# Kernel tuning notes

Hardware: AMD Instinct MI355X
Metric: run time of the kernel (lower is better)

The kernel has to match this reference:

```python
import jax, jax.numpy as jnp
import numpy as np

LN_EPS = 1e-3  # keras LayerNormalization default epsilon


def setup_inputs() -> dict:
    key = jax.random.key(0)
    ks = jax.random.split(key, 6)
    B, S, D, H, K = 4, 4096, 1024, 16, 64
    scale = 1.0 / np.sqrt(D)
    return {
        "x": jax.random.normal(ks[0], (B, S, D), jnp.float32),
        "Wq": jax.random.normal(ks[1], (D, H, K), jnp.float32) * scale,
        "bq": jnp.zeros((H, K), jnp.float32),
        "Wk": jax.random.normal(ks[2], (D, H, K), jnp.float32) * scale,
        "bk": jnp.zeros((H, K), jnp.float32),
        "Wv": jax.random.normal(ks[3], (D, H, K), jnp.float32) * scale,
        "bv": jnp.zeros((H, K), jnp.float32),
        "Wo": jax.random.normal(ks[4], (H, K, D), jnp.float32) * scale,
        "bo": jnp.zeros((D,), jnp.float32),
        "gamma": jnp.ones((D,), jnp.float32),
        "beta": jnp.zeros((D,), jnp.float32),
        "num_window": 8,
    }


def reference(x, Wq, bq, Wk, bk, Wv, bv, Wo, bo, gamma, beta, num_window):
    B, S, D = x.shape
    H, K = Wq.shape[1], Wq.shape[2]
    Sw = S // num_window
    # Block-diagonal (windowed) attention: reshape seq into windows instead of a Python loop.
    xw = x.reshape(B, num_window, Sw, D)  # [B, W, Sw, D]
    q = jnp.einsum('bwsd,dhk->bwshk', xw, Wq) + bq
    k = jnp.einsum('bwsd,dhk->bwshk', xw, Wk) + bk
    v = jnp.einsum('bwsd,dhk->bwshk', xw, Wv) + bv
    scores = jnp.einsum('bwqhk,bwshk->bwhqs', q, k) / jnp.sqrt(jnp.asarray(K, x.dtype))
    attn = jax.nn.softmax(scores, axis=-1)  # [B, W, H, Sw, Sw]
    ctx = jnp.einsum('bwhqs,bwshk->bwqhk', attn, v)
    attn_out = (jnp.einsum('bwqhk,hkd->bwqd', ctx, Wo) + bo).reshape(B, S, D)
    # residual + layernorm (keras eps=1e-3)
    y = x + attn_out
    mu = jnp.mean(y, axis=-1, keepdims=True)
    var = jnp.mean(jnp.square(y - mu), axis=-1, keepdims=True)
    return (y - mu) * jax.lax.rsqrt(var + LN_EPS) * gamma + beta
```

## Files before the change

kernel.cpp:

```cpp
#include <hip/hip_runtime.h>

typedef __bf16 bf16_t;
typedef __bf16 bf16x4 __attribute__((ext_vector_type(4)));
typedef __bf16 bf16x8 __attribute__((ext_vector_type(8)));
typedef float f32x4 __attribute__((ext_vector_type(4)));
typedef float f32x16 __attribute__((ext_vector_type(16)));

#define MFMA16(a, b, c) __builtin_amdgcn_mfma_f32_16x16x32_bf16((a), (b), (c), 0, 0, 0)
#define MFMA32(a, b, c) __builtin_amdgcn_mfma_f32_32x32x16_bf16((a), (b), (c), 0, 0, 0)

__device__ __forceinline__ void gl_lds16(const bf16_t* g, bf16_t* l) {
  __builtin_amdgcn_global_load_lds(
      (const __attribute__((address_space(1))) void*)g,
      (__attribute__((address_space(3))) void*)l, 16, 0, 0);
}

__global__ __launch_bounds__(256) void cast_x_kernel(const float* __restrict__ x,
                                                     bf16_t* __restrict__ xb) {
  size_t i = (size_t)blockIdx.x * 256 + threadIdx.x;
  float4 v = ((const float4*)x)[i];
  bf16x4 o = {(bf16_t)v.x, (bf16_t)v.y, (bf16_t)v.z, (bf16_t)v.w};
  ((bf16x4*)xb)[i] = o;
}

__global__ __launch_bounds__(256) void transpose_w_kernel(
    const float* __restrict__ Wq, const float* __restrict__ Wk,
    const float* __restrict__ Wv, const float* __restrict__ Wo,
    bf16_t* __restrict__ Wt, bf16_t* __restrict__ WoT) {
  __shared__ bf16_t T[64 * 68];
  const int z = blockIdx.z;
  const float* src = (z == 0) ? Wq : (z == 1) ? Wk : (z == 2) ? Wv : Wo;
  bf16_t* dst = (z < 3) ? (Wt + (size_t)z * 1024 * 1024) : WoT;
  const int tr = blockIdx.y * 64;
  const int tc = blockIdx.x * 64;
  const int tid = threadIdx.x;
#pragma unroll
  for (int it = 0; it < 4; ++it) {
    int t = tid + it * 256;
    int row = t >> 4, c4 = t & 15;
    float4 v = *(const float4*)&src[(size_t)(tr + row) * 1024 + tc + c4 * 4];
    bf16x4 o = {(bf16_t)v.x, (bf16_t)v.y, (bf16_t)v.z, (bf16_t)v.w};
    *(bf16x4*)&T[row * 68 + c4 * 4] = o;
  }
  __syncthreads();
#pragma unroll
  for (int it = 0; it < 2; ++it) {
    int t = tid + it * 256;
    int n = t >> 3, d8 = t & 7;
    bf16x8 o;
#pragma unroll
    for (int j = 0; j < 8; ++j) o[j] = T[(d8 * 8 + j) * 68 + n];
    *(bf16x8*)&dst[(size_t)(tc + n) * 1024 + tr + d8 * 8] = o;
  }
}

__global__ __launch_bounds__(256) void gemm_qkv_kernel(
    const bf16_t* __restrict__ A, const bf16_t* __restrict__ Bt,
    const float* __restrict__ bq, const float* __restrict__ bk,
    const float* __restrict__ bv, bf16_t* __restrict__ C) {
  __shared__ bf16_t As[128 * 64];
  __shared__ bf16_t Bs[128 * 64];
  const int tid = threadIdx.x;
  const int bm = blockIdx.y, bn = blockIdx.x;
  const int lane = tid & 63;
  const int l31 = lane & 31, lh = lane >> 5;
  const int wv = tid >> 6;
  const int wm = (wv & 1) * 64, wn = (wv >> 1) * 64;

  f32x16 acc[2][2];
#pragma unroll
  for (int i = 0; i < 2; ++i)
#pragma unroll
    for (int j = 0; j < 2; ++j)
#pragma unroll
      for (int e = 0; e < 16; ++e) acc[i][j][e] = 0.f;

  const bf16_t* Abase = A + (size_t)(bm * 128) * 1024;
  const bf16_t* Bbase = Bt + (size_t)(bn * 128) * 1024;

  for (int kt = 0; kt < 16; ++kt) {
    const int k0 = kt * 64;
#pragma unroll
    for (int i = 0; i < 4; ++i) {
      int t = tid + i * 256;
      int row = t >> 3;
      int g = (t & 7) ^ (row & 7);
      gl_lds16(Abase + (size_t)row * 1024 + k0 + g * 8, &As[t * 8]);
      gl_lds16(Bbase + (size_t)row * 1024 + k0 + g * 8, &Bs[t * 8]);
    }
    __syncthreads();
#pragma unroll
    for (int ks = 0; ks < 4; ++ks) {
      bf16x8 af[2], bfr[2];
#pragma unroll
      for (int mi = 0; mi < 2; ++mi) {
        int r = wm + mi * 32 + l31;
        af[mi] = *(const bf16x8*)&As[r * 64 + (((ks * 2 + lh) ^ (r & 7)) << 3)];
      }
#pragma unroll
      for (int ni = 0; ni < 2; ++ni) {
        int r = wn + ni * 32 + l31;
        bfr[ni] = *(const bf16x8*)&Bs[r * 64 + (((ks * 2 + lh) ^ (r & 7)) << 3)];
      }
#pragma unroll
      for (int mi = 0; mi < 2; ++mi)
#pragma unroll
        for (int ni = 0; ni < 2; ++ni)
          acc[mi][ni] = MFMA32(af[mi], bfr[ni], acc[mi][ni]);
    }
    __syncthreads();
  }

#pragma unroll
  for (int ni = 0; ni < 2; ++ni) {
    int col = bn * 128 + wn + ni * 32 + l31;
    float bias, scale;
    if (col < 1024) {
      bias = bq[col];
      scale = 0.125f;
    } else if (col < 2048) {
      bias = bk[col - 1024];
      scale = 1.f;
    } else {
      bias = bv[col - 2048];
      scale = 1.f;
    }
#pragma unroll
    for (int mi = 0; mi < 2; ++mi) {
      int rowb = bm * 128 + wm + mi * 32 + 4 * lh;
#pragma unroll
      for (int reg = 0; reg < 16; ++reg) {
        int row = rowb + (reg & 3) + 8 * (reg >> 2);
        C[(size_t)row * 3072 + col] = (bf16_t)((acc[mi][ni][reg] + bias) * scale);
      }
    }
  }
}

__global__ __launch_bounds__(256) void attn_kernel(
    const bf16_t* __restrict__ QKV, bf16_t* __restrict__ Ctx) {
  __shared__ bf16_t Ks[64 * 64];
  __shared__ bf16_t Vs[64 * 64];
  __shared__ bf16_t Pb[4][16 * 64];

  const int tid = threadIdx.x;
  const int wv = tid >> 6, quad = (tid >> 4) & 3, l15 = tid & 15;
  const int hid = blockIdx.x, qb = blockIdx.y;
  const int b = hid >> 7, w = (hid >> 4) & 7, h = hid & 15;
  const int rowW = b * 4096 + w * 512;
  const int qbase = qb * 128 + wv * 32;

  bf16x8 qf[2][2];
#pragma unroll
  for (int qt = 0; qt < 2; ++qt) {
    int rowQ = rowW + qbase + qt * 16 + l15;
#pragma unroll
    for (int kh = 0; kh < 2; ++kh)
      qf[qt][kh] = *(const bf16x8*)&QKV[(size_t)rowQ * 3072 + h * 64 + kh * 32 + quad * 8];
  }

  const bf16_t* Kb = QKV + (size_t)rowW * 3072 + 1024 + h * 64;
  const bf16_t* Vg = QKV + (size_t)rowW * 3072 + 2048 + h * 64;

  float lp[2] = {0.f, 0.f};
  f32x4 Oa[2][4];
  f32x4 zero = {0.f, 0.f, 0.f, 0.f};
#pragma unroll
  for (int qt = 0; qt < 2; ++qt)
#pragma unroll
    for (int dt = 0; dt < 4; ++dt) Oa[qt][dt] = zero;

  const int vrow = tid >> 2;
  const int vseg = tid & 3;

  for (int kt = 0; kt < 8; ++kt) {
#pragma unroll
    for (int i = 0; i < 2; ++i) {
      int t = tid + i * 256;
      int row = t >> 3;
      int g = (t & 7) ^ (row & 7);
      gl_lds16(Kb + (size_t)(kt * 64 + row) * 3072 + g * 8, &Ks[t * 8]);
    }
    {
      const bf16_t* src = Vg + (size_t)(kt * 64 + vrow) * 3072 + vseg * 16;
      bf16x8 v0 = *(const bf16x8*)&src[0];
      bf16x8 v1 = *(const bf16x8*)&src[8];
      int sg = vrow >> 3, sr = vrow & 7;
#pragma unroll
      for (int j = 0; j < 8; ++j) {
        int d0 = vseg * 16 + j;
        Vs[d0 * 64 + ((sg ^ (d0 & 7)) << 3) + sr] = v0[j];
        int d1 = vseg * 16 + 8 + j;
        Vs[d1 * 64 + ((sg ^ (d1 & 7)) << 3) + sr] = v1[j];
      }
    }
    __syncthreads();

    bf16x8 kf[4][2], vf[2][4];
#pragma unroll
    for (int jt = 0; jt < 4; ++jt) {
      int key = jt * 16 + l15;
#pragma unroll
      for (int kh = 0; kh < 2; ++kh)
        kf[jt][kh] = *(const bf16x8*)&Ks[key * 64 + (((kh * 4 + quad) ^ (key & 7)) << 3)];
    }
#pragma unroll
    for (int kh = 0; kh < 2; ++kh)
#pragma unroll
      for (int dt = 0; dt < 4; ++dt) {
        int d = dt * 16 + l15;
        vf[kh][dt] = *(const bf16x8*)&Vs[d * 64 + (((kh * 4 + quad) ^ (d & 7)) << 3)];
      }

#pragma unroll
    for (int qt = 0; qt < 2; ++qt) {
      f32x4 st[4];
#pragma unroll
      for (int jt = 0; jt < 4; ++jt) {
        f32x4 a = zero;
#pragma unroll
        for (int kh = 0; kh < 2; ++kh) a = MFMA16(kf[jt][kh], qf[qt][kh], a);
        st[jt] = a;
      }
      float ls = 0.f;
#pragma unroll
      for (int jt = 0; jt < 4; ++jt)
#pragma unroll
        for (int r = 0; r < 4; ++r) {
          float p = __expf(st[jt][r]);
          st[jt][r] = p;
          ls += p;
        }
      lp[qt] += ls;
#pragma unroll
      for (int jt = 0; jt < 4; ++jt) {
        bf16x4 pk = {(bf16_t)st[jt][0], (bf16_t)st[jt][1],
                     (bf16_t)st[jt][2], (bf16_t)st[jt][3]};
        int gs = (jt * 2 + (quad >> 1)) ^ (l15 & 7);
        *(bf16x4*)&Pb[wv][l15 * 64 + gs * 8 + (quad & 1) * 4] = pk;
      }
#pragma unroll
      for (int kh = 0; kh < 2; ++kh) {
        bf16x8 pf = *(const bf16x8*)&Pb[wv][l15 * 64 + (((kh * 4 + quad) ^ (l15 & 7)) << 3)];
#pragma unroll
        for (int dt = 0; dt < 4; ++dt) Oa[qt][dt] = MFMA16(pf, vf[kh][dt], Oa[qt][dt]);
      }
    }
    __syncthreads();
  }

#pragma unroll
  for (int qt = 0; qt < 2; ++qt) {
    float t = lp[qt];
    t += __shfl_xor(t, 16, 64);
    t += __shfl_xor(t, 32, 64);
    float inv_l = 1.0f / t;
    float inv[4];
#pragma unroll
    for (int r = 0; r < 4; ++r) inv[r] = __shfl(inv_l, quad * 4 + r, 64);
#pragma unroll
    for (int dt = 0; dt < 4; ++dt)
#pragma unroll
      for (int r = 0; r < 4; ++r) {
        int orow = rowW + qbase + qt * 16 + quad * 4 + r;
        Ctx[(size_t)orow * 1024 + h * 64 + dt * 16 + l15] = (bf16_t)(Oa[qt][dt][r] * inv[r]);
      }
  }
}

__global__ __launch_bounds__(256) void gemm_proj_kernel(
    const bf16_t* __restrict__ A, const bf16_t* __restrict__ Bt,
    const float* __restrict__ bo, const float* __restrict__ x,
    bf16_t* __restrict__ Yb) {
  __shared__ bf16_t As[128 * 64];
  __shared__ bf16_t Bs[128 * 64];
  const int tid = threadIdx.x;
  const int bm = blockIdx.y, bn = blockIdx.x;
  const int lane = tid & 63;
  const int l31 = lane & 31, lh = lane >> 5;
  const int wv = tid >> 6;
  const int wm = (wv & 1) * 64, wn = (wv >> 1) * 64;

  f32x16 acc[2][2];
#pragma unroll
  for (int i = 0; i < 2; ++i)
#pragma unroll
    for (int j = 0; j < 2; ++j)
#pragma unroll
      for (int e = 0; e < 16; ++e) acc[i][j][e] = 0.f;

  const bf16_t* Abase = A + (size_t)(bm * 128) * 1024;
  const bf16_t* Bbase = Bt + (size_t)(bn * 128) * 1024;

  for (int kt = 0; kt < 16; ++kt) {
    const int k0 = kt * 64;
#pragma unroll
    for (int i = 0; i < 4; ++i) {
      int t = tid + i * 256;
      int row = t >> 3;
      int g = (t & 7) ^ (row & 7);
      gl_lds16(Abase + (size_t)row * 1024 + k0 + g * 8, &As[t * 8]);
      gl_lds16(Bbase + (size_t)row * 1024 + k0 + g * 8, &Bs[t * 8]);
    }
    __syncthreads();
#pragma unroll
    for (int ks = 0; ks < 4; ++ks) {
      bf16x8 af[2], bfr[2];
#pragma unroll
      for (int mi = 0; mi < 2; ++mi) {
        int r = wm + mi * 32 + l31;
        af[mi] = *(const bf16x8*)&As[r * 64 + (((ks * 2 + lh) ^ (r & 7)) << 3)];
      }
#pragma unroll
      for (int ni = 0; ni < 2; ++ni) {
        int r = wn + ni * 32 + l31;
        bfr[ni] = *(const bf16x8*)&Bs[r * 64 + (((ks * 2 + lh) ^ (r & 7)) << 3)];
      }
#pragma unroll
      for (int mi = 0; mi < 2; ++mi)
#pragma unroll
        for (int ni = 0; ni < 2; ++ni)
          acc[mi][ni] = MFMA32(af[mi], bfr[ni], acc[mi][ni]);
    }
    __syncthreads();
  }

#pragma unroll
  for (int ni = 0; ni < 2; ++ni) {
    int col = bn * 128 + wn + ni * 32 + l31;
    float bias = bo[col];
#pragma unroll
    for (int mi = 0; mi < 2; ++mi) {
      int rowb = bm * 128 + wm + mi * 32 + 4 * lh;
#pragma unroll
      for (int reg = 0; reg < 16; ++reg) {
        int row = rowb + (reg & 3) + 8 * (reg >> 2);
        size_t idx = (size_t)row * 1024 + col;
        Yb[idx] = (bf16_t)(acc[mi][ni][reg] + bias + x[idx]);
      }
    }
  }
}

__global__ __launch_bounds__(256) void ln_kernel(const bf16_t* __restrict__ Yb,
                                                 float* __restrict__ Y,
                                                 const float* __restrict__ gamma,
                                                 const float* __restrict__ beta) {
  const int row = blockIdx.x, tid = threadIdx.x;
  bf16x4 yb = ((const bf16x4*)(Yb + (size_t)row * 1024))[tid];
  float y0 = (float)yb[0], y1 = (float)yb[1], y2 = (float)yb[2], y3 = (float)yb[3];
  float s = y0 + y1 + y2 + y3;
  float s2 = y0 * y0 + y1 * y1 + y2 * y2 + y3 * y3;
#pragma unroll
  for (int off = 1; off < 64; off <<= 1) {
    s += __shfl_xor(s, off, 64);
    s2 += __shfl_xor(s2, off, 64);
  }
  __shared__ float red[8];
  int wv = tid >> 6;
  if ((tid & 63) == 0) {
    red[wv] = s;
    red[4 + wv] = s2;
  }
  __syncthreads();
  s = red[0] + red[1] + red[2] + red[3];
  s2 = red[4] + red[5] + red[6] + red[7];
  float mean = s * (1.0f / 1024.0f);
  float var = s2 * (1.0f / 1024.0f) - mean * mean;
  float rs = rsqrtf(var + 1e-3f);
  float4 g = ((const float4*)gamma)[tid];
  float4 bb = ((const float4*)beta)[tid];
  float4 o;
  o.x = (y0 - mean) * rs * g.x + bb.x;
  o.y = (y1 - mean) * rs * g.y + bb.y;
  o.z = (y2 - mean) * rs * g.z + bb.z;
  o.w = (y3 - mean) * rs * g.w + bb.w;
  ((float4*)(Y + (size_t)row * 1024))[tid] = o;
}

extern "C" void kernel_launch(void* const* d_in, const int* in_sizes, int n_in,
                              void* d_out, int out_size, void* d_ws, size_t ws_size,
                              hipStream_t stream) {
  const float* x = (const float*)d_in[0];
  const float* Wq = (const float*)d_in[1];
  const float* bq = (const float*)d_in[2];
  const float* Wk = (const float*)d_in[3];
  const float* bk = (const float*)d_in[4];
  const float* Wv = (const float*)d_in[5];
  const float* bv = (const float*)d_in[6];
  const float* Wo = (const float*)d_in[7];
  const float* bo = (const float*)d_in[8];
  const float* gamma = (const float*)d_in[9];
  const float* beta = (const float*)d_in[10];
  float* Y = (float*)d_out;

  char* ws = (char*)d_ws;
  bf16_t* xb = (bf16_t*)(ws);
  bf16_t* Wt = (bf16_t*)(ws + 33554432);
  bf16_t* WoT = (bf16_t*)(ws + 39845888);
  bf16_t* QKVb = (bf16_t*)(ws + 41943040);
  bf16_t* Ctx = (bf16_t*)(ws + 142606336);
  bf16_t* Yb = (bf16_t*)(ws + 176160768);

  cast_x_kernel<<<16384, 256, 0, stream>>>(x, xb);
  transpose_w_kernel<<<dim3(16, 16, 4), 256, 0, stream>>>(Wq, Wk, Wv, Wo, Wt, WoT);
  gemm_qkv_kernel<<<dim3(24, 128), 256, 0, stream>>>(xb, Wt, bq, bk, bv, QKVb);
  attn_kernel<<<dim3(512, 4), 256, 0, stream>>>(QKVb, Ctx);
  gemm_proj_kernel<<<dim3(8, 128), 256, 0, stream>>>(Ctx, WoT, bo, x, Yb);
  ln_kernel<<<16384, 256, 0, stream>>>(Yb, Y, gamma, beta);
}
```

Measured before the change: 421.7 us.

## Rewrite QKV and projection GEMMs as 256x256 double-buffered pipelined tiles

Both GEMMs now use a shared 256x256-tile main loop run by 512 threads with 16x16 MFMAs. It double-buffers LDS, issuing global-to-LDS loads for the next k-slice interleaved with compute phases and using barriers, waitcnt and setprio. Block indices are swizzled to improve L2 reuse. The larger tile cuts global traffic per FLOP and hides load latency, at the cost of 128KB LDS and high register use, which lowers occupancy and leaves fewer blocks to cover the CUs.

```diff
diff --git a/kernel.cpp b/kernel.cpp
--- a/kernel.cpp
+++ b/kernel.cpp
@@ -4,10 +4,8 @@
 typedef __bf16 bf16x4 __attribute__((ext_vector_type(4)));
 typedef __bf16 bf16x8 __attribute__((ext_vector_type(8)));
 typedef float f32x4 __attribute__((ext_vector_type(4)));
-typedef float f32x16 __attribute__((ext_vector_type(16)));
 
 #define MFMA16(a, b, c) __builtin_amdgcn_mfma_f32_16x16x32_bf16((a), (b), (c), 0, 0, 0)
-#define MFMA32(a, b, c) __builtin_amdgcn_mfma_f32_32x32x16_bf16((a), (b), (c), 0, 0, 0)
 
 __device__ __forceinline__ void gl_lds16(const bf16_t* g, bf16_t* l) {
   __builtin_amdgcn_global_load_lds(
@@ -54,66 +52,157 @@
   }
 }
 
-__global__ __launch_bounds__(256) void gemm_qkv_kernel(
+
+__device__ __forceinline__ void stage_half(const bf16_t* __restrict__ g,
+                                           bf16_t* l, const int tid) {
+#pragma unroll
+  for (int j = 0; j < 2; ++j) {
+    int idx = j * 512 + tid;
+    int row = idx >> 3;
+    int c = (idx & 7) ^ (row & 7);
+    gl_lds16(g + (size_t)row * 1024 + c * 8, l + idx * 8);
+  }
+}
+
+__device__ __forceinline__ void gemm256_main(const bf16_t* __restrict__ Ab,
+                                             const bf16_t* __restrict__ Bb,
+                                             bf16_t* lds, f32x4 (&acc)[8][4],
+                                             const int tid) {
+  const int l15 = tid & 15, quad = (tid >> 4) & 3;
+  const int wv = tid >> 6, wm = wv >> 2, wn = wv & 3;
+  const int sx = l15 & 7;
+  const int brow0 = (wn & 1) * 64;
+
+  stage_half(Bb, lds + 2 * 8192, tid);
+  stage_half(Ab, lds + 0 * 8192, tid);
+  stage_half(Bb + 128 * 1024, lds + 3 * 8192, tid);
+  stage_half(Ab + 128 * 1024, lds + 1 * 8192, tid);
+  stage_half(Bb + 64, lds + 6 * 8192, tid);
+  stage_half(Ab + 64, lds + 4 * 8192, tid);
+  asm volatile("s_waitcnt vmcnt(4)" ::: "memory");
+  __builtin_amdgcn_s_barrier();
+
+  for (int t = 0; t < 16; ++t) {
+    bf16_t* const buf = lds + (t & 1) * 32768;
+    bf16_t* const nbuf = lds + ((t & 1) ^ 1) * 32768;
+    const bf16_t* const Ar = buf + wm * 8192;
+    const bf16_t* const Br = buf + (2 + (wn >> 1)) * 8192;
+
+    bf16x8 af[4][2], bfr[4][2];
+
+#pragma unroll
+    for (int mf = 0; mf < 4; ++mf)
+#pragma unroll
+      for (int ks = 0; ks < 2; ++ks)
+        af[mf][ks] = *(const bf16x8*)&Ar[(mf * 16 + l15) * 64 +
+                                         (((ks * 4 + quad) ^ sx) << 3)];
+#pragma unroll
+    for (int nf = 0; nf < 2; ++nf)
+#pragma unroll
+      for (int ks = 0; ks < 2; ++ks)
+        bfr[nf][ks] = *(const bf16x8*)&Br[(brow0 + nf * 16 + l15) * 64 +
+                                          (((ks * 4 + quad) ^ sx) << 3)];
+    if (t + 1 < 16) stage_half(Bb + 128 * 1024 + (t + 1) * 64, nbuf + 3 * 8192, tid);
+    __builtin_amdgcn_s_barrier();
+    asm volatile("s_waitcnt lgkmcnt(0)" ::: "memory");
+    __builtin_amdgcn_s_setprio(1);
+#pragma unroll
+    for (int mf = 0; mf < 4; ++mf)
+#pragma unroll
+      for (int nf = 0; nf < 2; ++nf)
+#pragma unroll
+        for (int ks = 0; ks < 2; ++ks)
+          acc[mf][nf] = MFMA16(af[mf][ks], bfr[nf][ks], acc[mf][nf]);
+    __builtin_amdgcn_s_setprio(0);
+    __builtin_amdgcn_s_barrier();
+
+#pragma unroll
+    for (int nf = 2; nf < 4; ++nf)
+#pragma unroll
+      for (int ks = 0; ks < 2; ++ks)
+        bfr[nf][ks] = *(const bf16x8*)&Br[(brow0 + nf * 16 + l15) * 64 +
+                                          (((ks * 4 + quad) ^ sx) << 3)];
+    if (t + 1 < 16) stage_half(Ab + 128 * 1024 + (t + 1) * 64, nbuf + 1 * 8192, tid);
+    __builtin_amdgcn_s_barrier();
+    asm volatile("s_waitcnt lgkmcnt(0)" ::: "memory");
+    __builtin_amdgcn_s_setprio(1);
+#pragma unroll
+    for (int mf = 0; mf < 4; ++mf)
+#pragma unroll
+      for (int nf = 2; nf < 4; ++nf)
+#pragma unroll
+        for (int ks = 0; ks < 2; ++ks)
+          acc[mf][nf] = MFMA16(af[mf][ks], bfr[nf][ks], acc[mf][nf]);
+    __builtin_amdgcn_s_setprio(0);
+    __builtin_amdgcn_s_barrier();
+
+#pragma unroll
+    for (int mf = 0; mf < 4; ++mf)
+#pragma unroll
+      for (int ks = 0; ks < 2; ++ks)
+        af[mf][ks] = *(const bf16x8*)&Ar[((mf + 4) * 16 + l15) * 64 +
+                                         (((ks * 4 + quad) ^ sx) << 3)];
+    if (t + 2 < 16) stage_half(Bb + (t + 2) * 64, buf + 2 * 8192, tid);
+    __builtin_amdgcn_s_barrier();
+    asm volatile("s_waitcnt lgkmcnt(0)" ::: "memory");
+    __builtin_amdgcn_s_setprio(1);
+#pragma unroll
+    for (int mf = 0; mf < 4; ++mf)
+#pragma unroll
+      for (int nf = 2; nf < 4; ++nf)
+#pragma unroll
+        for (int ks = 0; ks < 2; ++ks)
+          acc[mf + 4][nf] = MFMA16(af[mf][ks], bfr[nf][ks], acc[mf + 4][nf]);
+    __builtin_amdgcn_s_setprio(0);
+    __builtin_amdgcn_s_barrier();
+
+    if (t + 2 < 16) stage_half(Ab + (t + 2) * 64, buf + 0 * 8192, tid);
+    __builtin_amdgcn_s_barrier();
+    __builtin_amdgcn_s_setprio(1);
+#pragma unroll
+    for (int mf = 0; mf < 4; ++mf)
+#pragma unroll
+      for (int nf = 0; nf < 2; ++nf)
+#pragma unroll
+        for (int ks = 0; ks < 2; ++ks)
+          acc[mf + 4][nf] = MFMA16(af[mf][ks], bfr[nf][ks], acc[mf + 4][nf]);
+    __builtin_amdgcn_s_setprio(0);
+    if (t < 14)
+      asm volatile("s_waitcnt vmcnt(4)" ::: "memory");
+    else
+      asm volatile("s_waitcnt vmcnt(0)" ::: "memory");
+    __builtin_amdgcn_s_barrier();
+  }
+}
+
+__global__ __launch_bounds__(512) void gemm_qkv_kernel(
     const bf16_t* __restrict__ A, const bf16_t* __restrict__ Bt,
     const float* __restrict__ bq, const float* __restrict__ bk,
     const float* __restrict__ bv, bf16_t* __restrict__ C) {
-  __shared__ bf16_t As[128 * 64];
-  __shared__ bf16_t Bs[128 * 64];
+  __shared__ bf16_t lds[2 * 4 * 8192];
   const int tid = threadIdx.x;
-  const int bm = blockIdx.y, bn = blockIdx.x;
-  const int lane = tid & 63;
-  const int l31 = lane & 31, lh = lane >> 5;
-  const int wv = tid >> 6;
-  const int wm = (wv & 1) * 64, wn = (wv >> 1) * 64;
-
-  f32x16 acc[2][2];
-#pragma unroll
-  for (int i = 0; i < 2; ++i)
-#pragma unroll
-    for (int j = 0; j < 2; ++j)
-#pragma unroll
-      for (int e = 0; e < 16; ++e) acc[i][j][e] = 0.f;
-
-  const bf16_t* Abase = A + (size_t)(bm * 128) * 1024;
-  const bf16_t* Bbase = Bt + (size_t)(bn * 128) * 1024;
-
-  for (int kt = 0; kt < 16; ++kt) {
-    const int k0 = kt * 64;
-#pragma unroll
-    for (int i = 0; i < 4; ++i) {
-      int t = tid + i * 256;
-      int row = t >> 3;
-      int g = (t & 7) ^ (row & 7);
-      gl_lds16(Abase + (size_t)row * 1024 + k0 + g * 8, &As[t * 8]);
-      gl_lds16(Bbase + (size_t)row * 1024 + k0 + g * 8, &Bs[t * 8]);
-    }
-    __syncthreads();
-#pragma unroll
-    for (int ks = 0; ks < 4; ++ks) {
-      bf16x8 af[2], bfr[2];
-#pragma unroll
-      for (int mi = 0; mi < 2; ++mi) {
-        int r = wm + mi * 32 + l31;
-        af[mi] = *(const bf16x8*)&As[r * 64 + (((ks * 2 + lh) ^ (r & 7)) << 3)];
-      }
-#pragma unroll
-      for (int ni = 0; ni < 2; ++ni) {
-        int r = wn + ni * 32 + l31;
-        bfr[ni] = *(const bf16x8*)&Bs[r * 64 + (((ks * 2 + lh) ^ (r & 7)) << 3)];
-      }
-#pragma unroll
-      for (int mi = 0; mi < 2; ++mi)
-#pragma unroll
-        for (int ni = 0; ni < 2; ++ni)
-          acc[mi][ni] = MFMA32(af[mi], bfr[ni], acc[mi][ni]);
-    }
-    __syncthreads();
-  }
-
-#pragma unroll
-  for (int ni = 0; ni < 2; ++ni) {
-    int col = bn * 128 + wn + ni * 32 + l31;
+  const int lin = blockIdx.x;
+  const int swz = (lin & 7) * 96 + (lin >> 3);
+  const int bm = swz / 12, bn = swz - bm * 12;
+
+  f32x4 acc[8][4];
+#pragma unroll
+  for (int i = 0; i < 8; ++i)
+#pragma unroll
+    for (int j = 0; j < 4; ++j)
+#pragma unroll
+      for (int e = 0; e < 4; ++e) acc[i][j][e] = 0.f;
+
+  gemm256_main(A + (size_t)(bm * 256) * 1024, Bt + (size_t)(bn * 256) * 1024,
+               lds, acc, tid);
+
+  const int l15 = tid & 15, quad = (tid >> 4) & 3;
+  const int wv = tid >> 6, wm = wv >> 2, wn = wv & 3;
+  const int row0 = bm * 256 + wm * 128 + quad * 4;
+  const int col0 = bn * 256 + wn * 64;
+#pragma unroll
+  for (int nf = 0; nf < 4; ++nf) {
+    int col = col0 + nf * 16 + l15;
     float bias, scale;
     if (col < 1024) {
       bias = bq[col];
@@ -126,14 +215,12 @@
       scale = 1.f;
     }
 #pragma unroll
-    for (int mi = 0; mi < 2; ++mi) {
-      int rowb = bm * 128 + wm + mi * 32 + 4 * lh;
-#pragma unroll
-      for (int reg = 0; reg < 16; ++reg) {
-        int row = rowb + (reg & 3) + 8 * (reg >> 2);
-        C[(size_t)row * 3072 + col] = (bf16_t)((acc[mi][ni][reg] + bias) * scale);
-      }
-    }
+    for (int mf = 0; mf < 8; ++mf)
+#pragma unroll
+      for (int r = 0; r < 4; ++r) {
+        int row = row0 + mf * 16 + r;
+        C[(size_t)row * 3072 + col] = (bf16_t)((acc[mf][nf][r] + bias) * scale);
+      }
   }
 }
 
@@ -268,77 +355,43 @@
   }
 }
 
-__global__ __launch_bounds__(256) void gemm_proj_kernel(
+__global__ __launch_bounds__(512) void gemm_proj_kernel(
     const bf16_t* __restrict__ A, const bf16_t* __restrict__ Bt,
     const float* __restrict__ bo, const float* __restrict__ x,
     bf16_t* __restrict__ Yb) {
-  __shared__ bf16_t As[128 * 64];
-  __shared__ bf16_t Bs[128 * 64];
+  __shared__ bf16_t lds[2 * 4 * 8192];
   const int tid = threadIdx.x;
-  const int bm = blockIdx.y, bn = blockIdx.x;
-  const int lane = tid & 63;
-  const int l31 = lane & 31, lh = lane >> 5;
-  const int wv = tid >> 6;
-  const int wm = (wv & 1) * 64, wn = (wv >> 1) * 64;
-
-  f32x16 acc[2][2];
-#pragma unroll
-  for (int i = 0; i < 2; ++i)
-#pragma unroll
-    for (int j = 0; j < 2; ++j)
-#pragma unroll
-      for (int e = 0; e < 16; ++e) acc[i][j][e] = 0.f;
-
-  const bf16_t* Abase = A + (size_t)(bm * 128) * 1024;
-  const bf16_t* Bbase = Bt + (size_t)(bn * 128) * 1024;
-
-  for (int kt = 0; kt < 16; ++kt) {
-    const int k0 = kt * 64;
-#pragma unroll
-    for (int i = 0; i < 4; ++i) {
-      int t = tid + i * 256;
-      int row = t >> 3;
-      int g = (t & 7) ^ (row & 7);
-      gl_lds16(Abase + (size_t)row * 1024 + k0 + g * 8, &As[t * 8]);
-      gl_lds16(Bbase + (size_t)row * 1024 + k0 + g * 8, &Bs[t * 8]);
-    }
-    __syncthreads();
-#pragma unroll
-    for (int ks = 0; ks < 4; ++ks) {
-      bf16x8 af[2], bfr[2];
-#pragma unroll
-      for (int mi = 0; mi < 2; ++mi) {
-        int r = wm + mi * 32 + l31;
-        af[mi] = *(const bf16x8*)&As[r * 64 + (((ks * 2 + lh) ^ (r & 7)) << 3)];
-      }
-#pragma unroll
-      for (int ni = 0; ni < 2; ++ni) {
-        int r = wn + ni * 32 + l31;
-        bfr[ni] = *(const bf16x8*)&Bs[r * 64 + (((ks * 2 + lh) ^ (r & 7)) << 3)];
-      }
-#pragma unroll
-      for (int mi = 0; mi < 2; ++mi)
-#pragma unroll
-        for (int ni = 0; ni < 2; ++ni)
-          acc[mi][ni] = MFMA32(af[mi], bfr[ni], acc[mi][ni]);
-    }
-    __syncthreads();
-  }
-
-#pragma unroll
-  for (int ni = 0; ni < 2; ++ni) {
-    int col = bn * 128 + wn + ni * 32 + l31;
+  const int lin = blockIdx.x;
+  const int swz = (lin & 7) * 32 + (lin >> 3);
+  const int bm = swz >> 2, bn = swz & 3;
+
+  f32x4 acc[8][4];
+#pragma unroll
+  for (int i = 0; i < 8; ++i)
+#pragma unroll
+    for (int j = 0; j < 4; ++j)
+#pragma unroll
+      for (int e = 0; e < 4; ++e) acc[i][j][e] = 0.f;
+
+  gemm256_main(A + (size_t)(bm * 256) * 1024, Bt + (size_t)(bn * 256) * 1024,
+               lds, acc, tid);
+
+  const int l15 = tid & 15, quad = (tid >> 4) & 3;
+  const int wv = tid >> 6, wm = wv >> 2, wn = wv & 3;
+  const int row0 = bm * 256 + wm * 128 + quad * 4;
+  const int col0 = bn * 256 + wn * 64;
+#pragma unroll
+  for (int nf = 0; nf < 4; ++nf) {
+    int col = col0 + nf * 16 + l15;
     float bias = bo[col];
 #pragma unroll
-    for (int mi = 0; mi < 2; ++mi) {
-      int rowb = bm * 128 + wm + mi * 32 + 4 * lh;
-#pragma unroll
-      for (int reg = 0; reg < 16; ++reg) {
-        int row = rowb + (reg & 3) + 8 * (reg >> 2);
+    for (int mf = 0; mf < 8; ++mf)
+#pragma unroll
+      for (int r = 0; r < 4; ++r) {
+        int row = row0 + mf * 16 + r;
         size_t idx = (size_t)row * 1024 + col;
-        Yb[idx] = (bf16_t)(acc[mi][ni][reg] + bias + x[idx]);
-      }
-    }
+        Yb[idx] = (bf16_t)(acc[mf][nf][r] + bias + x[idx]);
+      }
   }
 }
 
@@ -404,8 +457,8 @@
 
   cast_x_kernel<<<16384, 256, 0, stream>>>(x, xb);
   transpose_w_kernel<<<dim3(16, 16, 4), 256, 0, stream>>>(Wq, Wk, Wv, Wo, Wt, WoT);
-  gemm_qkv_kernel<<<dim3(24, 128), 256, 0, stream>>>(xb, Wt, bq, bk, bv, QKVb);
+  gemm_qkv_kernel<<<768, 512, 0, stream>>>(xb, Wt, bq, bk, bv, QKVb);
   attn_kernel<<<dim3(512, 4), 256, 0, stream>>>(QKVb, Ctx);
-  gemm_proj_kernel<<<dim3(8, 128), 256, 0, stream>>>(Ctx, WoT, bo, x, Yb);
+  gemm_proj_kernel<<<256, 512, 0, stream>>>(Ctx, WoT, bo, x, Yb);
   ln_kernel<<<16384, 256, 0, stream>>>(Yb, Y, gamma, beta);
 }
```

Result: no change. 420.2 us (-0.4%).
